# Optimization experiments

Measured on AMD Instinct MI355X. Metric: run time of the kernel, lower is better.

## Reference

```python
import jax, jax.numpy as jnp
import numpy as np

NQ = 10
EDGES = [[0, 1], [1, 2], [2, 3], [3, 4], [4, 5], [5, 6], [6, 7], [7, 8], [8, 9], [9, 0]]
RANGE = 2  # StronglyEntanglingLayers ranges=[2]
CRX_ANGLE = np.pi / 3.0  # trainBool=False -> constant angle

_c, _s = np.cos(CRX_ANGLE / 2), np.sin(CRX_ANGLE / 2)
CRX = np.array([[1, 0, 0, 0], [0, 1, 0, 0], [0, 0, _c, -1j * _s], [0, 0, -1j * _s, _c]], dtype=np.complex64)
CNOT = np.array([[1, 0, 0, 0], [0, 1, 0, 0], [0, 0, 0, 1], [0, 0, 1, 0]], dtype=np.complex64)


def _apply_1q(state, U, w):
    # state: (B, 2, ..., 2); U: (2,2) or batched (B,2,2)
    st = jnp.moveaxis(state, 1 + w, -1)
    if U.ndim == 3:
        st = jnp.einsum('b...i,bji->b...j', st, U)
    else:
        st = jnp.einsum('...i,ji->...j', st, U)
    return jnp.moveaxis(st, -1, 1 + w)


def _apply_2q(state, U, w1, w2):
    st = jnp.moveaxis(state, (1 + w1, 1 + w2), (-2, -1))
    shp = st.shape
    st = st.reshape(shp[:-2] + (4,))
    st = jnp.einsum('...i,ji->...j', st, U)
    return jnp.moveaxis(st.reshape(shp), (-2, -1), (1 + w1, 1 + w2))


def _ry_batch(theta):
    # per-sample RY gates, theta: (B,) -> (B,2,2)
    c, s = jnp.cos(theta / 2), jnp.sin(theta / 2)
    U = jnp.stack([jnp.stack([c, -s], -1), jnp.stack([s, c], -1)], -2)
    return U.astype(jnp.complex64)


def _rot(phi, theta, omega):
    # qml.Rot = RZ(omega) RY(theta) RZ(phi)
    c, s = jnp.cos(theta / 2), jnp.sin(theta / 2)
    u00 = jnp.exp(-0.5j * (phi + omega)) * c
    u01 = -jnp.exp(0.5j * (phi - omega)) * s
    u10 = jnp.exp(-0.5j * (phi - omega)) * s
    u11 = jnp.exp(0.5j * (phi + omega)) * c
    return jnp.stack([jnp.stack([u00, u01]), jnp.stack([u10, u11])]).astype(jnp.complex64)


def _circuit(inputs, weights):
    B = inputs.shape[0]
    state = jnp.zeros((B,) + (2,) * NQ, jnp.complex64)
    state = state.at[(slice(None),) + (0,) * NQ].set(1.0)
    # AngleEmbedding(rotation='Y')
    for w in range(NQ):
        state = _apply_1q(state, _ry_batch(inputs[:, w]), w)
    # CRX entanglers over the chain graph, angle pi/3
    for a, b in EDGES:
        state = _apply_2q(state, CRX, a, b)
    # StronglyEntanglingLayers, n_layers = weights.shape[0] = 1, range 2
    for l in range(weights.shape[0]):
        for i in range(NQ):
            state = _apply_1q(state, _rot(weights[l, i, 0], weights[l, i, 1], weights[l, i, 2]), i)
        for i in range(NQ):
            state = _apply_2q(state, CNOT, i, (i + RANGE) % NQ)
    # expval(PauliZ(i)) for each wire
    probs = state.real ** 2 + state.imag ** 2
    exps = []
    for i in range(NQ):
        axes = tuple(a for a in range(1, NQ + 1) if a != 1 + i)
        marg = probs.sum(axis=axes)  # (B, 2)
        exps.append(marg[:, 0] - marg[:, 1])
    return jnp.stack(exps, -1)  # (B, NQ)


def setup_inputs() -> dict:
    key = jax.random.key(0)
    k1, k2 = jax.random.split(key)
    inputs = jax.random.normal(k1, (8192, NQ), dtype=jnp.float32)
    weights = jax.random.uniform(k2, (1, NQ, 3), dtype=jnp.float32, minval=0.0, maxval=2 * np.pi)
    return {"inputs": inputs, "weights": weights}


def reference(inputs, weights):
    return _circuit(inputs, weights)
```

## Files before the change

kernel.cpp:

```cpp
#include <hip/hip_runtime.h>

#define NQ 10

typedef float f32x2 __attribute__((ext_vector_type(2)));
struct cplx2 { f32x2 x, y; };

template<int M>
__device__ __forceinline__ void plswap1(float v, float &A, float &B){
    if constexpr (M == 16) {
        auto r = __builtin_amdgcn_permlane16_swap(__float_as_uint(v), __float_as_uint(v), false, false);
        A = __uint_as_float(r[0]); B = __uint_as_float(r[1]);
    } else {
        auto r = __builtin_amdgcn_permlane32_swap(__float_as_uint(v), __float_as_uint(v), false, false);
        A = __uint_as_float(r[0]); B = __uint_as_float(r[1]);
    }
}
template<int M>
__device__ __forceinline__ void plswap2(f32x2 v, f32x2 &A, f32x2 &B){
    float ax, bx, ay, by;
    plswap1<M>(v.x, ax, bx);
    plswap1<M>(v.y, ay, by);
    A.x = ax; A.y = ay;
    B.x = bx; B.y = by;
}

template<int M>
__device__ __forceinline__ float lxf(float v){
    if constexpr (M == 1 || M == 2 || M == 8) {
        constexpr int ctrl = (M == 1) ? 0xB1 : (M == 2) ? 0x4E : 0x128;
        return __int_as_float(__builtin_amdgcn_update_dpp(
            0, __float_as_int(v), ctrl, 0xF, 0xF, true));
    } else if constexpr (M == 4) {
        float up = __int_as_float(__builtin_amdgcn_update_dpp(
            0, __float_as_int(v), 0x104, 0xF, 0xF, true));
        float dn = __int_as_float(__builtin_amdgcn_update_dpp(
            0, __float_as_int(v), 0x114, 0xF, 0xF, true));
        return (threadIdx.x & 4) ? dn : up;
    } else {
        float A, Bv; plswap1<M>(v, A, Bv);
        return (threadIdx.x & M) ? A : Bv;
    }
}
template<int M>
__device__ __forceinline__ f32x2 lx2(f32x2 v){
    f32x2 r; r.x = lxf<M>(v.x); r.y = lxf<M>(v.y); return r;
}
template<int M>
__device__ __forceinline__ cplx2 lxc(cplx2 a){
    cplx2 r; r.x = lx2<M>(a.x); r.y = lx2<M>(a.y); return r;
}

template<int M, int R>
__device__ __forceinline__ void ry_reg(cplx2 (&a)[16], float c, float s){
    if constexpr (R < 16) {
        if constexpr ((R & M) == 0) {
            cplx2 a0 = a[R], a1 = a[R|M];
            a[R].x   = c*a0.x - s*a1.x;  a[R].y   = c*a0.y - s*a1.y;
            a[R|M].x = s*a0.x + c*a1.x;  a[R|M].y = s*a0.y + c*a1.y;
        }
        ry_reg<M,R+1>(a, c, s);
    }
}

template<int LM, int R>
__device__ __forceinline__ void ry_lane(cplx2 (&a)[16], float c, float se){
    if constexpr (R < 16) {
        cplx2 p = lxc<LM>(a[R]);
        cplx2 m = a[R];
        a[R].x = c*m.x + se*p.x;
        a[R].y = c*m.y + se*p.y;
        ry_lane<LM,R+1>(a, c, se);
    }
}

template<int M, int R>
__device__ __forceinline__ void ry_lane_pl(cplx2 (&a)[16], float kA, float kB){
    if constexpr (R < 16) {
        f32x2 Ax,Bx,Ay,By;
        plswap2<M>(a[R].x, Ax, Bx);
        plswap2<M>(a[R].y, Ay, By);
        a[R].x = kA*Ax + kB*Bx;
        a[R].y = kA*Ay + kB*By;
        ry_lane_pl<M,R+1>(a, kA, kB);
    }
}


template<int MC, int MT, int R>
__device__ __forceinline__ void crx_rr(cplx2 (&a)[16], float cc, float ss){
    if constexpr (R < 16) {
        if constexpr ((R & MC) != 0 && (R & MT) == 0) {
            cplx2 a0 = a[R], a1 = a[R|MT];
            a[R].x    = cc*a0.x + ss*a1.y;  a[R].y    = cc*a0.y - ss*a1.x;
            a[R|MT].x = cc*a1.x + ss*a0.y;  a[R|MT].y = cc*a1.y - ss*a0.x;
        }
        crx_rr<MC,MT,R+1>(a, cc, ss);
    }
}

template<int MC, int LM, int R>
__device__ __forceinline__ void crx_rl(cplx2 (&a)[16], float cc, float ss){
    if constexpr (R < 16) {
        if constexpr ((R & MC) != 0) {
            cplx2 p = lxc<LM>(a[R]);
            cplx2 m = a[R];
            a[R].x = cc*m.x + ss*p.y;
            a[R].y = cc*m.y - ss*p.x;
        }
        crx_rl<MC,LM,R+1>(a, cc, ss);
    }
}

template<int MT, int R>
__device__ __forceinline__ void crx_lr(cplx2 (&a)[16], float al, float be){
    if constexpr (R < 16) {
        if constexpr ((R & MT) == 0) {
            cplx2 a0 = a[R], a1 = a[R|MT];
            a[R].x    = al*a0.x + be*a1.y;  a[R].y    = al*a0.y - be*a1.x;
            a[R|MT].x = al*a1.x + be*a0.y;  a[R|MT].y = al*a1.y - be*a0.x;
        }
        crx_lr<MT,R+1>(a, al, be);
    }
}

template<int TLM, int R>
__device__ __forceinline__ void crx_ll(cplx2 (&a)[16], float al, float be){
    if constexpr (R < 16) {
        cplx2 p = lxc<TLM>(a[R]);
        cplx2 m = a[R];
        a[R].x = al*m.x + be*p.y;
        a[R].y = al*m.y - be*p.x;
        crx_ll<TLM,R+1>(a, al, be);
    }
}

template<int M, int R>
__device__ __forceinline__ void crx_ll_pl(cplx2 (&a)[16],
        float kmA,float kmB,float kpA,float kpB){
    if constexpr (R < 16) {
        f32x2 Ax,Bx,Ay,By;
        plswap2<M>(a[R].x, Ax, Bx);
        plswap2<M>(a[R].y, Ay, By);
        a[R].x = kmA*Ax + kmB*Bx + kpA*Ay + kpB*By;
        a[R].y = kmA*Ay + kmB*By - kpA*Ax - kpB*Bx;
        crx_ll_pl<M,R+1>(a, kmA,kmB,kpA,kpB);
    }
}

template<int I>
__device__ __forceinline__ void do_ry(cplx2 (&amp)[16], int lane, const float* __restrict__ w){
    float c, s;
    __sincosf(0.5f * w[I*3 + 1], &s, &c);
    if constexpr (I < 4) {
        ry_reg<(1<<I),0>(amp, c, s);
    } else if constexpr (I < 8) {
        constexpr int LM = 1 << (I - 4);
        const bool hi = (lane & LM) != 0;
        ry_lane<LM,0>(amp, c, hi ? s : -s);
    } else {
        constexpr int LM = 1 << (I - 4);
        const bool hi = (lane & LM) != 0;
        ry_lane_pl<LM,0>(amp, hi ? s : c, hi ? c : -s);
    }
}

template<int R>
__device__ __forceinline__ void accum4(const cplx2 (&a)[16], f32x2 &SA, f32x2 &SB, f32x2 &SC, f32x2 &SD){
    if constexpr (R < 16) {
        f32x2 p = a[R].x*a[R].x + a[R].y*a[R].y;
        SA += ((R>>2) & 1)            ? -p : p;
        SB += ((R>>3) & 1)            ? -p : p;
        SC += ((R ^ (R>>2)) & 1)      ? -p : p;
        SD += (((R>>1) ^ (R>>3)) & 1) ? -p : p;
        accum4<R+1>(a, SA, SB, SC, SD);
    }
}

__device__ __forceinline__ f32x2 wave_sum2(f32x2 v){
    v += lx2< 1>(v);
    v += lx2< 2>(v);
    v += lx2< 4>(v);
    v += lx2< 8>(v);
    f32x2 A, B;
    plswap2<16>(v, A, B); v = A + B;
    plswap2<32>(v, A, B); v = A + B;
    return v;
}

__device__ __forceinline__ f32x2 wht2(f32x2 v, int lane){
    f32x2 p;
    p = lx2< 1>(v); v = (lane &  1) ? p - v : v + p;
    p = lx2< 2>(v); v = (lane &  2) ? p - v : v + p;
    p = lx2< 4>(v); v = (lane &  4) ? p - v : v + p;
    p = lx2< 8>(v); v = (lane &  8) ? p - v : v + p;
    f32x2 A, B;
    plswap2<16>(v, A, B); v = (lane & 16) ? A - B : A + B;
    plswap2<32>(v, A, B); v = (lane & 32) ? A - B : A + B;
    return v;
}

__device__ __forceinline__ f32x2 fsgn2(f32x2 v, unsigned s){
    f32x2 r;
    r.x = __uint_as_float(__float_as_uint(v.x) ^ s);
    r.y = __uint_as_float(__float_as_uint(v.y) ^ s);
    return r;
}
__device__ __forceinline__ unsigned parsgn(int lane, int m){
    return (unsigned)((__builtin_popcount(lane & m) & 1)) << 31;
}

__global__ __launch_bounds__(256, 4) void qsim_kernel(const float* __restrict__ inputs,
                                                      const float* __restrict__ weights,
                                                      float* __restrict__ out, int B, int nPairs){
    const int lane = threadIdx.x & 63;
    const int pair = __builtin_amdgcn_readfirstlane((int)((blockIdx.x * blockDim.x + threadIdx.x) >> 6));
    if (pair >= nPairs) return;

    const int s0 = 2 * pair;
    const int s1 = (s0 + 1 < B) ? s0 + 1 : s0;
    const float* ang0 = inputs + (size_t)s0 * NQ;
    const float* ang1 = inputs + (size_t)s1 * NQ;

    f32x2 F = 1.f;
    #pragma unroll
    for (int w = 4; w < NQ; ++w) {
        float sA, cA, sB, cB;
        __sincosf(0.5f * ang0[w], &sA, &cA);
        __sincosf(0.5f * ang1[w], &sB, &cB);
        bool hi = (lane & (1 << (w - 4))) != 0;
        f32x2 f; f.x = hi ? sA : cA; f.y = hi ? sB : cB;
        F *= f;
    }

    f32x2 c[4], s[4];
    #pragma unroll
    for (int w = 0; w < 4; ++w) {
        float sA, cA, sB, cB;
        __sincosf(0.5f * ang0[w], &sA, &cA);
        __sincosf(0.5f * ang1[w], &sB, &cB);
        c[w].x = cA; c[w].y = cB; s[w].x = sA; s[w].y = sB;
    }

    f32x2 v2a = F * c[0], v2b = F * s[0];
    f32x2 v4[4] = { v2a*c[1], v2b*c[1], v2a*s[1], v2b*s[1] };
    f32x2 v8[8] = { v4[0]*c[2], v4[1]*c[2], v4[2]*c[2], v4[3]*c[2],
                    v4[0]*s[2], v4[1]*s[2], v4[2]*s[2], v4[3]*s[2] };

    cplx2 amp[16];
    #pragma unroll
    for (int r = 0; r < 8; ++r) {
        amp[r].x   = v8[r] * c[3]; amp[r].y   = 0.f;
        amp[r+8].x = v8[r] * s[3]; amp[r+8].y = 0.f;
    }

    const float cc = 0.86602540378443864676f;
    const float ss = 0.5f;
    crx_rr<1, 2, 0>(amp, cc, ss);
    crx_rr<2, 4, 0>(amp, cc, ss);
    crx_rr<4, 8, 0>(amp, cc, ss);
    crx_rl<8, 1, 0>(amp, cc, ss);
    { bool t = (lane &  1); crx_ll< 2,0>(amp, t?cc:1.f, t?ss:0.f); }
    { bool t = (lane &  2); crx_ll< 4,0>(amp, t?cc:1.f, t?ss:0.f); }
    { bool t = (lane &  4); crx_ll< 8,0>(amp, t?cc:1.f, t?ss:0.f); }
    { bool t = (lane &  8); bool bt = (lane & 16);
      float al = t?cc:1.f, be = t?ss:0.f;
      crx_ll_pl<16,0>(amp, bt?0.f:al, bt?al:0.f, bt?be:0.f, bt?0.f:be); }
    { bool t = (lane & 16); bool bt = (lane & 32);
      float al = t?cc:1.f, be = t?ss:0.f;
      crx_ll_pl<32,0>(amp, bt?0.f:al, bt?al:0.f, bt?be:0.f, bt?0.f:be); }
    { bool t = (lane & 32); crx_lr< 1,0>(amp, t?cc:1.f, t?ss:0.f); }

    {
        float cp[NQ], sp[NQ];
        #pragma unroll
        for (int i = 0; i < NQ; ++i)
            __sincosf(0.5f * weights[i*3 + 0], &sp[i], &cp[i]);

        float Lr = 1.f, Li = 0.f;
        #pragma unroll
        for (int wq = 4; wq < NQ; ++wq) {
            float sg = (lane & (1 << (wq - 4))) ? sp[wq] : -sp[wq];
            float nr = Lr*cp[wq] - Li*sg;
            float ni = Li*cp[wq] + Lr*sg;
            Lr = nr; Li = ni;
        }

        float er[8], ei[8];
        er[0] = Lr; ei[0] = Li;
        #pragma unroll
        for (int q = 0; q < 3; ++q) {
            const int n = 1 << q;
            #pragma unroll
            for (int r = n - 1; r >= 0; --r) {
                float ar = er[r], ai = ei[r];
                er[r+n] = ar*cp[q] - ai*sp[q];
                ei[r+n] = ai*cp[q] + ar*sp[q];
                er[r]   = ar*cp[q] + ai*sp[q];
                ei[r]   = ai*cp[q] - ar*sp[q];
            }
        }
        #pragma unroll
        for (int r = 0; r < 8; ++r) {
            float g0r = er[r]*cp[3] + ei[r]*sp[3], g0i = ei[r]*cp[3] - er[r]*sp[3];
            float g1r = er[r]*cp[3] - ei[r]*sp[3], g1i = ei[r]*cp[3] + er[r]*sp[3];
            f32x2 x, y;
            x = amp[r].x;   y = amp[r].y;
            amp[r].x   = x*g0r - y*g0i;  amp[r].y   = y*g0r + x*g0i;
            x = amp[r+8].x; y = amp[r+8].y;
            amp[r+8].x = x*g1r - y*g1i;  amp[r+8].y = y*g1r + x*g1i;
        }
    }

    do_ry<0>(amp, lane, weights);
    do_ry<1>(amp, lane, weights);
    do_ry<2>(amp, lane, weights);
    do_ry<3>(amp, lane, weights);
    do_ry<4>(amp, lane, weights);
    do_ry<5>(amp, lane, weights);
    do_ry<6>(amp, lane, weights);
    do_ry<7>(amp, lane, weights);
    do_ry<8>(amp, lane, weights);
    do_ry<9>(amp, lane, weights);

    f32x2 SA = 0.f, SB = 0.f, SC = 0.f, SD = 0.f;
    accum4<0>(amp, SA, SB, SC, SD);

    f32x2 r0  = wave_sum2(fsgn2(SA, parsgn(lane, 21)));
    f32x2 r1  = wave_sum2(fsgn2(SB, parsgn(lane, 42)));
    f32x2 wsc = wht2(SC, lane);
    f32x2 wsd = wht2(SD, lane);

    float* o0 = out + (size_t)s0 * NQ;
    const bool has1 = (s0 + 1 < B);
    float* o1 = out + (size_t)(s0 + 1) * NQ;

    if (lane == 0) {
        o0[0] = r0.x; o0[1] = r1.x; o0[2] = wsc.x; o0[3] = wsd.x;
        if (has1) { o1[0] = r0.y; o1[1] = r1.y; o1[2] = wsc.y; o1[3] = wsd.y; }
    } else if (lane == 1) {
        o0[4] = wsc.x; if (has1) o1[4] = wsc.y;
    } else if (lane == 5) {
        o0[6] = wsc.x; if (has1) o1[6] = wsc.y;
    } else if (lane == 21) {
        o0[8] = wsc.x; if (has1) o1[8] = wsc.y;
    } else if (lane == 2) {
        o0[5] = wsd.x; if (has1) o1[5] = wsd.y;
    } else if (lane == 10) {
        o0[7] = wsd.x; if (has1) o1[7] = wsd.y;
    } else if (lane == 42) {
        o0[9] = wsd.x; if (has1) o1[9] = wsd.y;
    }
}

extern "C" void kernel_launch(void* const* d_in, const int* in_sizes, int n_in,
                              void* d_out, int out_size, void* d_ws, size_t ws_size,
                              hipStream_t stream) {
    const float* inputs  = (const float*)d_in[0];
    const float* weights = (const float*)d_in[1];
    float* out = (float*)d_out;
    const int B = in_sizes[0] / NQ;
    const int nPairs = (B + 1) / 2;
    const int wavesPerBlock = 256 / 64;
    const int blocks = (nPairs + wavesPerBlock - 1) / wavesPerBlock;
    qsim_kernel<<<blocks, 256, 0, stream>>>(inputs, weights, out, B, nPairs);
}
```

Measured before the change: 80.22 us.

## Process one sample per wavefront instead of two packed samples

Replaces the two-samples-per-wave packed f32x2 layout with one sample per wave using scalar floats. Each wave now simulates a single 1024-amplitude state, which halves register use per wave and doubles the number of waves launched. Packed FMA throughput (v_pk_fma) is given up, and the cross-lane DPP and permlane traffic is paid once per sample instead of being shared across two samples.

```diff
diff --git a/kernel.cpp b/kernel.cpp
--- a/kernel.cpp
+++ b/kernel.cpp
@@ -2,8 +2,7 @@
 
 #define NQ 10
 
-typedef float f32x2 __attribute__((ext_vector_type(2)));
-struct cplx2 { f32x2 x, y; };
+struct cplx { float x, y; };
 
 template<int M>
 __device__ __forceinline__ void plswap1(float v, float &A, float &B){
@@ -14,14 +13,6 @@
         auto r = __builtin_amdgcn_permlane32_swap(__float_as_uint(v), __float_as_uint(v), false, false);
         A = __uint_as_float(r[0]); B = __uint_as_float(r[1]);
     }
-}
-template<int M>
-__device__ __forceinline__ void plswap2(f32x2 v, f32x2 &A, f32x2 &B){
-    float ax, bx, ay, by;
-    plswap1<M>(v.x, ax, bx);
-    plswap1<M>(v.y, ay, by);
-    A.x = ax; A.y = ay;
-    B.x = bx; B.y = by;
 }
 
 template<int M>
@@ -42,19 +33,15 @@
     }
 }
 template<int M>
-__device__ __forceinline__ f32x2 lx2(f32x2 v){
-    f32x2 r; r.x = lxf<M>(v.x); r.y = lxf<M>(v.y); return r;
-}
-template<int M>
-__device__ __forceinline__ cplx2 lxc(cplx2 a){
-    cplx2 r; r.x = lx2<M>(a.x); r.y = lx2<M>(a.y); return r;
+__device__ __forceinline__ cplx lxc(cplx a){
+    cplx r; r.x = lxf<M>(a.x); r.y = lxf<M>(a.y); return r;
 }
 
 template<int M, int R>
-__device__ __forceinline__ void ry_reg(cplx2 (&a)[16], float c, float s){
+__device__ __forceinline__ void ry_reg(cplx (&a)[16], float c, float s){
     if constexpr (R < 16) {
         if constexpr ((R & M) == 0) {
-            cplx2 a0 = a[R], a1 = a[R|M];
+            cplx a0 = a[R], a1 = a[R|M];
             a[R].x   = c*a0.x - s*a1.x;  a[R].y   = c*a0.y - s*a1.y;
             a[R|M].x = s*a0.x + c*a1.x;  a[R|M].y = s*a0.y + c*a1.y;
         }
@@ -63,10 +50,10 @@
 }
 
 template<int LM, int R>
-__device__ __forceinline__ void ry_lane(cplx2 (&a)[16], float c, float se){
-    if constexpr (R < 16) {
-        cplx2 p = lxc<LM>(a[R]);
-        cplx2 m = a[R];
+__device__ __forceinline__ void ry_lane(cplx (&a)[16], float c, float se){
+    if constexpr (R < 16) {
+        cplx p = lxc<LM>(a[R]);
+        cplx m = a[R];
         a[R].x = c*m.x + se*p.x;
         a[R].y = c*m.y + se*p.y;
         ry_lane<LM,R+1>(a, c, se);
@@ -74,11 +61,11 @@
 }
 
 template<int M, int R>
-__device__ __forceinline__ void ry_lane_pl(cplx2 (&a)[16], float kA, float kB){
-    if constexpr (R < 16) {
-        f32x2 Ax,Bx,Ay,By;
-        plswap2<M>(a[R].x, Ax, Bx);
-        plswap2<M>(a[R].y, Ay, By);
+__device__ __forceinline__ void ry_lane_pl(cplx (&a)[16], float kA, float kB){
+    if constexpr (R < 16) {
+        float Ax,Bx,Ay,By;
+        plswap1<M>(a[R].x, Ax, Bx);
+        plswap1<M>(a[R].y, Ay, By);
         a[R].x = kA*Ax + kB*Bx;
         a[R].y = kA*Ay + kB*By;
         ry_lane_pl<M,R+1>(a, kA, kB);
@@ -87,10 +74,10 @@
 
 
 template<int MC, int MT, int R>
-__device__ __forceinline__ void crx_rr(cplx2 (&a)[16], float cc, float ss){
+__device__ __forceinline__ void crx_rr(cplx (&a)[16], float cc, float ss){
     if constexpr (R < 16) {
         if constexpr ((R & MC) != 0 && (R & MT) == 0) {
-            cplx2 a0 = a[R], a1 = a[R|MT];
+            cplx a0 = a[R], a1 = a[R|MT];
             a[R].x    = cc*a0.x + ss*a1.y;  a[R].y    = cc*a0.y - ss*a1.x;
             a[R|MT].x = cc*a1.x + ss*a0.y;  a[R|MT].y = cc*a1.y - ss*a0.x;
         }
@@ -99,11 +86,11 @@
 }
 
 template<int MC, int LM, int R>
-__device__ __forceinline__ void crx_rl(cplx2 (&a)[16], float cc, float ss){
+__device__ __forceinline__ void crx_rl(cplx (&a)[16], float cc, float ss){
     if constexpr (R < 16) {
         if constexpr ((R & MC) != 0) {
-            cplx2 p = lxc<LM>(a[R]);
-            cplx2 m = a[R];
+            cplx p = lxc<LM>(a[R]);
+            cplx m = a[R];
             a[R].x = cc*m.x + ss*p.y;
             a[R].y = cc*m.y - ss*p.x;
         }
@@ -112,10 +99,10 @@
 }
 
 template<int MT, int R>
-__device__ __forceinline__ void crx_lr(cplx2 (&a)[16], float al, float be){
+__device__ __forceinline__ void crx_lr(cplx (&a)[16], float al, float be){
     if constexpr (R < 16) {
         if constexpr ((R & MT) == 0) {
-            cplx2 a0 = a[R], a1 = a[R|MT];
+            cplx a0 = a[R], a1 = a[R|MT];
             a[R].x    = al*a0.x + be*a1.y;  a[R].y    = al*a0.y - be*a1.x;
             a[R|MT].x = al*a1.x + be*a0.y;  a[R|MT].y = al*a1.y - be*a0.x;
         }
@@ -124,10 +111,10 @@
 }
 
 template<int TLM, int R>
-__device__ __forceinline__ void crx_ll(cplx2 (&a)[16], float al, float be){
-    if constexpr (R < 16) {
-        cplx2 p = lxc<TLM>(a[R]);
-        cplx2 m = a[R];
+__device__ __forceinline__ void crx_ll(cplx (&a)[16], float al, float be){
+    if constexpr (R < 16) {
+        cplx p = lxc<TLM>(a[R]);
+        cplx m = a[R];
         a[R].x = al*m.x + be*p.y;
         a[R].y = al*m.y - be*p.x;
         crx_ll<TLM,R+1>(a, al, be);
@@ -135,12 +122,12 @@
 }
 
 template<int M, int R>
-__device__ __forceinline__ void crx_ll_pl(cplx2 (&a)[16],
+__device__ __forceinline__ void crx_ll_pl(cplx (&a)[16],
         float kmA,float kmB,float kpA,float kpB){
     if constexpr (R < 16) {
-        f32x2 Ax,Bx,Ay,By;
-        plswap2<M>(a[R].x, Ax, Bx);
-        plswap2<M>(a[R].y, Ay, By);
+        float Ax,Bx,Ay,By;
+        plswap1<M>(a[R].x, Ax, Bx);
+        plswap1<M>(a[R].y, Ay, By);
         a[R].x = kmA*Ax + kmB*Bx + kpA*Ay + kpB*By;
         a[R].y = kmA*Ay + kmB*By - kpA*Ax - kpB*Bx;
         crx_ll_pl<M,R+1>(a, kmA,kmB,kpA,kpB);
@@ -148,7 +135,7 @@
 }
 
 template<int I>
-__device__ __forceinline__ void do_ry(cplx2 (&amp)[16], int lane, const float* __restrict__ w){
+__device__ __forceinline__ void do_ry(cplx (&amp)[16], int lane, const float* __restrict__ w){
     float c, s;
     __sincosf(0.5f * w[I*3 + 1], &s, &c);
     if constexpr (I < 4) {
@@ -165,9 +152,9 @@
 }
 
 template<int R>
-__device__ __forceinline__ void accum4(const cplx2 (&a)[16], f32x2 &SA, f32x2 &SB, f32x2 &SC, f32x2 &SD){
-    if constexpr (R < 16) {
-        f32x2 p = a[R].x*a[R].x + a[R].y*a[R].y;
+__device__ __forceinline__ void accum4(const cplx (&a)[16], float &SA, float &SB, float &SC, float &SD){
+    if constexpr (R < 16) {
+        float p = a[R].x*a[R].x + a[R].y*a[R].y;
         SA += ((R>>2) & 1)            ? -p : p;
         SB += ((R>>3) & 1)            ? -p : p;
         SC += ((R ^ (R>>2)) & 1)      ? -p : p;
@@ -176,34 +163,31 @@
     }
 }
 
-__device__ __forceinline__ f32x2 wave_sum2(f32x2 v){
-    v += lx2< 1>(v);
-    v += lx2< 2>(v);
-    v += lx2< 4>(v);
-    v += lx2< 8>(v);
-    f32x2 A, B;
-    plswap2<16>(v, A, B); v = A + B;
-    plswap2<32>(v, A, B); v = A + B;
+__device__ __forceinline__ float wave_sum1(float v){
+    v += lxf< 1>(v);
+    v += lxf< 2>(v);
+    v += lxf< 4>(v);
+    v += lxf< 8>(v);
+    float A, B;
+    plswap1<16>(v, A, B); v = A + B;
+    plswap1<32>(v, A, B); v = A + B;
     return v;
 }
 
-__device__ __forceinline__ f32x2 wht2(f32x2 v, int lane){
-    f32x2 p;
-    p = lx2< 1>(v); v = (lane &  1) ? p - v : v + p;
-    p = lx2< 2>(v); v = (lane &  2) ? p - v : v + p;
-    p = lx2< 4>(v); v = (lane &  4) ? p - v : v + p;
-    p = lx2< 8>(v); v = (lane &  8) ? p - v : v + p;
-    f32x2 A, B;
-    plswap2<16>(v, A, B); v = (lane & 16) ? A - B : A + B;
-    plswap2<32>(v, A, B); v = (lane & 32) ? A - B : A + B;
+__device__ __forceinline__ float wht1(float v, int lane){
+    float p;
+    p = lxf< 1>(v); v = (lane &  1) ? p - v : v + p;
+    p = lxf< 2>(v); v = (lane &  2) ? p - v : v + p;
+    p = lxf< 4>(v); v = (lane &  4) ? p - v : v + p;
+    p = lxf< 8>(v); v = (lane &  8) ? p - v : v + p;
+    float A, B;
+    plswap1<16>(v, A, B); v = (lane & 16) ? A - B : A + B;
+    plswap1<32>(v, A, B); v = (lane & 32) ? A - B : A + B;
     return v;
 }
 
-__device__ __forceinline__ f32x2 fsgn2(f32x2 v, unsigned s){
-    f32x2 r;
-    r.x = __uint_as_float(__float_as_uint(v.x) ^ s);
-    r.y = __uint_as_float(__float_as_uint(v.y) ^ s);
-    return r;
+__device__ __forceinline__ float fsgn1(float v, unsigned s){
+    return __uint_as_float(__float_as_uint(v) ^ s);
 }
 __device__ __forceinline__ unsigned parsgn(int lane, int m){
     return (unsigned)((__builtin_popcount(lane & m) & 1)) << 31;
@@ -211,42 +195,32 @@
 
 __global__ __launch_bounds__(256, 4) void qsim_kernel(const float* __restrict__ inputs,
                                                       const float* __restrict__ weights,
-                                                      float* __restrict__ out, int B, int nPairs){
+                                                      float* __restrict__ out, int B){
     const int lane = threadIdx.x & 63;
-    const int pair = __builtin_amdgcn_readfirstlane((int)((blockIdx.x * blockDim.x + threadIdx.x) >> 6));
-    if (pair >= nPairs) return;
-
-    const int s0 = 2 * pair;
-    const int s1 = (s0 + 1 < B) ? s0 + 1 : s0;
-    const float* ang0 = inputs + (size_t)s0 * NQ;
-    const float* ang1 = inputs + (size_t)s1 * NQ;
-
-    f32x2 F = 1.f;
+    const int smp = __builtin_amdgcn_readfirstlane((int)((blockIdx.x * blockDim.x + threadIdx.x) >> 6));
+    if (smp >= B) return;
+
+    const float* ang = inputs + (size_t)smp * NQ;
+
+    float F = 1.f;
     #pragma unroll
     for (int w = 4; w < NQ; ++w) {
-        float sA, cA, sB, cB;
-        __sincosf(0.5f * ang0[w], &sA, &cA);
-        __sincosf(0.5f * ang1[w], &sB, &cB);
-        bool hi = (lane & (1 << (w - 4))) != 0;
-        f32x2 f; f.x = hi ? sA : cA; f.y = hi ? sB : cB;
-        F *= f;
-    }
-
-    f32x2 c[4], s[4];
+        float sA, cA;
+        __sincosf(0.5f * ang[w], &sA, &cA);
+        F *= (lane & (1 << (w - 4))) ? sA : cA;
+    }
+
+    float c[4], s[4];
     #pragma unroll
-    for (int w = 0; w < 4; ++w) {
-        float sA, cA, sB, cB;
-        __sincosf(0.5f * ang0[w], &sA, &cA);
-        __sincosf(0.5f * ang1[w], &sB, &cB);
-        c[w].x = cA; c[w].y = cB; s[w].x = sA; s[w].y = sB;
-    }
-
-    f32x2 v2a = F * c[0], v2b = F * s[0];
-    f32x2 v4[4] = { v2a*c[1], v2b*c[1], v2a*s[1], v2b*s[1] };
-    f32x2 v8[8] = { v4[0]*c[2], v4[1]*c[2], v4[2]*c[2], v4[3]*c[2],
+    for (int w = 0; w < 4; ++w)
+        __sincosf(0.5f * ang[w], &s[w], &c[w]);
+
+    float v2a = F * c[0], v2b = F * s[0];
+    float v4[4] = { v2a*c[1], v2b*c[1], v2a*s[1], v2b*s[1] };
+    float v8[8] = { v4[0]*c[2], v4[1]*c[2], v4[2]*c[2], v4[3]*c[2],
                     v4[0]*s[2], v4[1]*s[2], v4[2]*s[2], v4[3]*s[2] };
 
-    cplx2 amp[16];
+    cplx amp[16];
     #pragma unroll
     for (int r = 0; r < 8; ++r) {
         amp[r].x   = v8[r] * c[3]; amp[r].y   = 0.f;
@@ -303,7 +277,7 @@
         for (int r = 0; r < 8; ++r) {
             float g0r = er[r]*cp[3] + ei[r]*sp[3], g0i = ei[r]*cp[3] - er[r]*sp[3];
             float g1r = er[r]*cp[3] - ei[r]*sp[3], g1i = ei[r]*cp[3] + er[r]*sp[3];
-            f32x2 x, y;
+            float x, y;
             x = amp[r].x;   y = amp[r].y;
             amp[r].x   = x*g0r - y*g0i;  amp[r].y   = y*g0r + x*g0i;
             x = amp[r+8].x; y = amp[r+8].y;
@@ -322,33 +296,29 @@
     do_ry<8>(amp, lane, weights);
     do_ry<9>(amp, lane, weights);
 
-    f32x2 SA = 0.f, SB = 0.f, SC = 0.f, SD = 0.f;
+    float SA = 0.f, SB = 0.f, SC = 0.f, SD = 0.f;
     accum4<0>(amp, SA, SB, SC, SD);
 
-    f32x2 r0  = wave_sum2(fsgn2(SA, parsgn(lane, 21)));
-    f32x2 r1  = wave_sum2(fsgn2(SB, parsgn(lane, 42)));
-    f32x2 wsc = wht2(SC, lane);
-    f32x2 wsd = wht2(SD, lane);
-
-    float* o0 = out + (size_t)s0 * NQ;
-    const bool has1 = (s0 + 1 < B);
-    float* o1 = out + (size_t)(s0 + 1) * NQ;
-
+    float r0  = wave_sum1(fsgn1(SA, parsgn(lane, 21)));
+    float r1  = wave_sum1(fsgn1(SB, parsgn(lane, 42)));
+    float wsc = wht1(SC, lane);
+    float wsd = wht1(SD, lane);
+
+    float* o = out + (size_t)smp * NQ;
     if (lane == 0) {
-        o0[0] = r0.x; o0[1] = r1.x; o0[2] = wsc.x; o0[3] = wsd.x;
-        if (has1) { o1[0] = r0.y; o1[1] = r1.y; o1[2] = wsc.y; o1[3] = wsd.y; }
+        o[0] = r0; o[1] = r1; o[2] = wsc; o[3] = wsd;
     } else if (lane == 1) {
-        o0[4] = wsc.x; if (has1) o1[4] = wsc.y;
+        o[4] = wsc;
     } else if (lane == 5) {
-        o0[6] = wsc.x; if (has1) o1[6] = wsc.y;
+        o[6] = wsc;
     } else if (lane == 21) {
-        o0[8] = wsc.x; if (has1) o1[8] = wsc.y;
+        o[8] = wsc;
     } else if (lane == 2) {
-        o0[5] = wsd.x; if (has1) o1[5] = wsd.y;
+        o[5] = wsd;
     } else if (lane == 10) {
-        o0[7] = wsd.x; if (has1) o1[7] = wsd.y;
+        o[7] = wsd;
     } else if (lane == 42) {
-        o0[9] = wsd.x; if (has1) o1[9] = wsd.y;
+        o[9] = wsd;
     }
 }
 
@@ -359,8 +329,7 @@
     const float* weights = (const float*)d_in[1];
     float* out = (float*)d_out;
     const int B = in_sizes[0] / NQ;
-    const int nPairs = (B + 1) / 2;
     const int wavesPerBlock = 256 / 64;
-    const int blocks = (nPairs + wavesPerBlock - 1) / wavesPerBlock;
-    qsim_kernel<<<blocks, 256, 0, stream>>>(inputs, weights, out, B, nPairs);
-}
+    const int blocks = (B + wavesPerBlock - 1) / wavesPerBlock;
+    qsim_kernel<<<blocks, 256, 0, stream>>>(inputs, weights, out, B);
+}
```

Result: slower. 86.34 us (+7.6%).
